# Optimization experiments

Measured on AMD Instinct MI355X. Metric: run time of the kernel, lower is better.

Reference implementation:

```python
import jax, jax.numpy as jnp
import numpy as np

E, K, H, F = 16, 4, 1024, 2048
SL, BS = 2048, 2
ALPHA, LIMIT = 1.702, 7.0
CAPACITY_FACTOR = 1.0


def setup_inputs() -> dict:
    key = jax.random.key(0)
    ks = jax.random.split(key, 7)
    x = jax.random.normal(ks[0], (SL, BS, H), jnp.float32)
    router_weight = jax.random.normal(ks[1], (E, H), jnp.float32) * 0.02
    router_bias = jax.random.normal(ks[2], (E,), jnp.float32) * 0.02
    w1 = jax.random.normal(ks[3], (E, H, 2 * F), jnp.float32) * 0.02
    w2 = jax.random.normal(ks[4], (E, F, H), jnp.float32) * 0.02
    w1_bias = jax.random.normal(ks[5], (E, 2 * F), jnp.float32) * 0.02
    w2_bias = jax.random.normal(ks[6], (E, H), jnp.float32) * 0.02
    return {"x": x, "router_weight": router_weight, "router_bias": router_bias,
            "w1": w1, "w2": w2, "w1_bias": w1_bias, "w2_bias": w2_bias}


def reference(x, router_weight, router_bias, w1, w2, w1_bias, w2_bias):
    sl, bs, h = x.shape
    T = sl * bs                      # total tokens
    N = T * K                        # total routed copies
    C = int(CAPACITY_FACTOR * K * T / E)  # static expert capacity
    xf = x.reshape(T, h)

    # --- route_tokens ---
    logits = xf @ router_weight.T + router_bias            # [T, E]
    expert_weights, expert_indices = jax.lax.top_k(logits, K)  # [T, K]
    expert_weights = jax.nn.softmax(expert_weights, axis=-1)
    router_scores = jnp.zeros_like(logits).at[
        jnp.arange(T)[:, None], expert_indices].set(expert_weights).T  # [E, T]

    # --- indices_and_bins: stable sort by expert + histogram ---
    te = expert_indices.reshape(-1)                        # [N] expert id per copy
    ew = expert_weights.reshape(-1)                        # [N] weight per copy
    order = jnp.argsort(te)                                # stable sort -> permutation
    tokens_per_expert = jnp.zeros((E,), jnp.int32).at[te].add(1)
    starts = jnp.cumsum(tokens_per_expert) - tokens_per_expert  # exclusive cumsum

    # --- binned_gather: [E, C, H], overflow tokens dropped, underfull slots zero ---
    j = jnp.arange(C)
    pos = starts[:, None] + j[None, :]                     # [E, C] position in sorted order
    valid = j[None, :] < tokens_per_expert[:, None]        # [E, C]
    flat_idx = order[jnp.clip(pos, 0, N - 1)]              # [E, C] index into flattened copies
    tok = flat_idx // K                                    # [E, C] source token row
    xb = jnp.where(valid[..., None], xf[tok], 0.0)         # [E, C, H]

    # --- mlp_forward: interleaved GLU ---
    gate_up = jnp.einsum('ech,ehf->ecf', xb, w1) + w1_bias[:, None, :]  # [E, C, 2F]
    gate = jnp.minimum(gate_up[..., ::2], LIMIT)
    up = jnp.clip(gate_up[..., 1::2], -LIMIT, LIMIT)
    glu = gate * jax.nn.sigmoid(gate * ALPHA)
    y = jnp.einsum('ecf,efh->ech', (up + 1.0) * glu, w2) + w2_bias[:, None, :]  # [E, C, H]

    # --- binned_scatter: weighted combine back to token rows ---
    w = jnp.where(valid, ew[flat_idx], 0.0)                # [E, C]
    out = jnp.zeros((T, h), x.dtype).at[tok.reshape(-1)].add(
        (w[..., None] * y).reshape(-1, h))
    return out.reshape(sl, bs, h), expert_weights, router_scores
```

## Files before the change

kernel.cpp:

```cpp
#include <hip/hip_runtime.h>
#include <hip/hip_bf16.h>

#define T_TOK 4096
#define E_EXP 16
#define TOPK 4
#define HDIM 1024
#define FDIM 2048
#define CAP 1024
#define NCOPY (T_TOK*TOPK)

typedef __bf16 bf16x8 __attribute__((ext_vector_type(8)));
typedef __bf16 bf16x4 __attribute__((ext_vector_type(4)));
typedef float  f32x4  __attribute__((ext_vector_type(4)));

__global__ __launch_bounds__(64) void router_kernel(
    const float* __restrict__ x, const float* __restrict__ rw, const float* __restrict__ rb,
    float* __restrict__ ew_out, float* __restrict__ rs_out, int* __restrict__ te_out)
{
    int t = blockIdx.x;
    int lane = threadIdx.x;
    const float* xr = x + (size_t)t * HDIM;
    float xv[16];
#pragma unroll
    for (int i = 0; i < 16; ++i) xv[i] = xr[i * 64 + lane];
    float lg[E_EXP];
#pragma unroll
    for (int e = 0; e < E_EXP; ++e) {
        const float* wrow = rw + (size_t)e * HDIM;
        float s = 0.f;
#pragma unroll
        for (int i = 0; i < 16; ++i) s += xv[i] * wrow[i * 64 + lane];
#pragma unroll
        for (int off = 32; off > 0; off >>= 1) s += __shfl_xor(s, off, 64);
        lg[e] = s + rb[e];
    }
    int mask = 0; float vals[4]; int idxs[4];
#pragma unroll
    for (int k = 0; k < 4; ++k) {
        float m = -3.4e38f; int a = 0;
#pragma unroll
        for (int e = 0; e < E_EXP; ++e) {
            bool take = (((mask >> e) & 1) == 0) && (lg[e] > m);
            m = take ? lg[e] : m;
            a = take ? e : a;
        }
        vals[k] = m; idxs[k] = a; mask |= (1 << a);
    }
    float wk[4]; float ssum = 0.f;
#pragma unroll
    for (int k = 0; k < 4; ++k) { wk[k] = __expf(vals[k] - vals[0]); ssum += wk[k]; }
    float inv = 1.f / ssum;
#pragma unroll
    for (int k = 0; k < 4; ++k) wk[k] *= inv;
    if (lane < 4) {
        float wv = 0.f; int iv = 0;
#pragma unroll
        for (int k = 0; k < 4; ++k) if (lane == k) { wv = wk[k]; iv = idxs[k]; }
        ew_out[t * 4 + lane] = wv;
        te_out[t * 4 + lane] = iv;
    }
    if (lane < E_EXP) {
        float v = 0.f;
#pragma unroll
        for (int k = 0; k < 4; ++k) v = (idxs[k] == lane) ? wk[k] : v;
        rs_out[(size_t)lane * T_TOK + t] = v;
    }
}

__global__ __launch_bounds__(256) void binning_kernel(
    const int* __restrict__ te, const float* __restrict__ ew,
    int* __restrict__ slot_tok, float* __restrict__ slot_w)
{
    __shared__ int cnt[256][17];
    int tid = threadIdx.x;
#pragma unroll
    for (int e = 0; e < E_EXP; ++e) cnt[tid][e] = 0;
    __syncthreads();
    int base = tid * 64;
    for (int i = 0; i < 64; ++i) cnt[tid][te[base + i]]++;
    __syncthreads();
    if (tid < E_EXP) {
        int run = 0;
        for (int t2 = 0; t2 < 256; ++t2) { int v = cnt[t2][tid]; cnt[t2][tid] = run; run += v; }
    }
    __syncthreads();
    for (int s = tid; s < E_EXP * CAP; s += 256) { slot_tok[s] = -1; slot_w[s] = 0.f; }
    __syncthreads();
    for (int i = 0; i < 64; ++i) {
        int idx = base + i;
        int e = te[idx];
        int r = cnt[tid][e]; cnt[tid][e] = r + 1;
        if (r < CAP) { slot_tok[e * CAP + r] = idx >> 2; slot_w[e * CAP + r] = ew[idx]; }
    }
}

__global__ __launch_bounds__(256) void gather_kernel(
    const float* __restrict__ x, const int* __restrict__ slot_tok, __bf16* __restrict__ xg)
{
    int s = blockIdx.x, tid = threadIdx.x;
    int tok = slot_tok[s];
    bf16x4 o;
    if (tok >= 0) {
        float4 v = *(const float4*)(x + (size_t)tok * HDIM + tid * 4);
        o[0] = (__bf16)v.x; o[1] = (__bf16)v.y; o[2] = (__bf16)v.z; o[3] = (__bf16)v.w;
    } else {
        o[0] = (__bf16)0.f; o[1] = (__bf16)0.f; o[2] = (__bf16)0.f; o[3] = (__bf16)0.f;
    }
    *(bf16x4*)(xg + (size_t)s * HDIM + tid * 4) = o;
}

__global__ __launch_bounds__(256) void transpose_cvt_kernel(
    const float* __restrict__ in, __bf16* __restrict__ out, int R, int Cc, int tilesR, int tilesC)
{
    __shared__ __bf16 tile[64][68];
    int bx = blockIdx.x;
    int tpe = tilesR * tilesC;
    int e = bx / tpe; int rem = bx - e * tpe;
    int tr = rem / tilesC; int tc = rem - tr * tilesC;
    const float* ine = in + (size_t)e * R * Cc;
    __bf16* oute = out + (size_t)e * R * Cc;
    int r0 = tr * 64, c0 = tc * 64;
    int tid = threadIdx.x;
    int rr = tid >> 4, c4 = (tid & 15) << 2;
#pragma unroll
    for (int it = 0; it < 4; ++it) {
        int r = rr + it * 16;
        float4 v = *(const float4*)(ine + (size_t)(r0 + r) * Cc + c0 + c4);
        tile[r][c4 + 0] = (__bf16)v.x; tile[r][c4 + 1] = (__bf16)v.y;
        tile[r][c4 + 2] = (__bf16)v.z; tile[r][c4 + 3] = (__bf16)v.w;
    }
    __syncthreads();
#pragma unroll
    for (int it = 0; it < 4; ++it) {
        int c = rr + it * 16;
        bf16x4 o;
        o[0] = tile[c4 + 0][c]; o[1] = tile[c4 + 1][c];
        o[2] = tile[c4 + 2][c]; o[3] = tile[c4 + 3][c];
        *(bf16x4*)(oute + (size_t)(c0 + c) * R + r0 + c4) = o;
    }
}

__global__ __launch_bounds__(256) void zero_kernel(float4* p)
{
    p[(size_t)blockIdx.x * 256 + threadIdx.x] = make_float4(0.f, 0.f, 0.f, 0.f);
}

template <int EPI>
__global__ __launch_bounds__(256) void gemm_kernel(
    const __bf16* __restrict__ A, const __bf16* __restrict__ Bt, const float* __restrict__ bias,
    __bf16* __restrict__ actout, float* __restrict__ out,
    const int* __restrict__ slot_tok, const float* __restrict__ slot_w,
    int Kd, int tilesM, int tilesN, int N)
{
    __shared__ __bf16 at[128 * 32];
    __shared__ __bf16 bts[128 * 32];
    int bx = blockIdx.x;
    int tpe = tilesM * tilesN;
    int e = bx / tpe; int rem = bx - e * tpe;
    int bm = rem / tilesN; int bn = rem - bm * tilesN;
    const __bf16* Ab = A + (size_t)e * 1024 * Kd + (size_t)(bm * 128) * Kd;
    const __bf16* Bb = Bt + (size_t)e * N * Kd + (size_t)(bn * 128) * Kd;
    int tid = threadIdx.x;
    int c0 = tid, c1 = tid + 256;
    int ar0 = c0 >> 2, ak0 = (c0 & 3) << 3;
    int ar1 = c1 >> 2, ak1 = (c1 & 3) << 3;

    uint4 ra0 = *(const uint4*)(Ab + (size_t)ar0 * Kd + ak0);
    uint4 ra1 = *(const uint4*)(Ab + (size_t)ar1 * Kd + ak1);
    uint4 rb0 = *(const uint4*)(Bb + (size_t)ar0 * Kd + ak0);
    uint4 rb1 = *(const uint4*)(Bb + (size_t)ar1 * Kd + ak1);

    f32x4 zero4 = {0.f, 0.f, 0.f, 0.f};
    f32x4 acc[4][4];
#pragma unroll
    for (int mi = 0; mi < 4; ++mi)
#pragma unroll
        for (int ni = 0; ni < 4; ++ni) acc[mi][ni] = zero4;

    int w = tid >> 6, l = tid & 63;
    int q = l >> 4, ln = l & 15;
    int wr = (w >> 1) << 6, wc = (w & 1) << 6;

    for (int k0 = 0; k0 < Kd; k0 += 32) {
        *(uint4*)(at + c0 * 8) = ra0;
        *(uint4*)(at + c1 * 8) = ra1;
        *(uint4*)(bts + c0 * 8) = rb0;
        *(uint4*)(bts + c1 * 8) = rb1;
        int kn = k0 + 32;
        if (kn < Kd) {
            ra0 = *(const uint4*)(Ab + (size_t)ar0 * Kd + kn + ak0);
            ra1 = *(const uint4*)(Ab + (size_t)ar1 * Kd + kn + ak1);
            rb0 = *(const uint4*)(Bb + (size_t)ar0 * Kd + kn + ak0);
            rb1 = *(const uint4*)(Bb + (size_t)ar1 * Kd + kn + ak1);
        }
        __syncthreads();
        bf16x8 af[4], bfr[4];
#pragma unroll
        for (int mi = 0; mi < 4; ++mi)
            af[mi] = *(const bf16x8*)(at + (wr + mi * 16 + ln) * 32 + q * 8);
#pragma unroll
        for (int ni = 0; ni < 4; ++ni)
            bfr[ni] = *(const bf16x8*)(bts + (wc + ni * 16 + ln) * 32 + q * 8);
#pragma unroll
        for (int mi = 0; mi < 4; ++mi)
#pragma unroll
            for (int ni = 0; ni < 4; ++ni)
                acc[mi][ni] = __builtin_amdgcn_mfma_f32_16x16x32_bf16(af[mi], bfr[ni], acc[mi][ni], 0, 0, 0);
        __syncthreads();
    }

    float bv[4];
#pragma unroll
    for (int ni = 0; ni < 4; ++ni) bv[ni] = bias[(size_t)e * N + bn * 128 + wc + ni * 16 + ln];

    if constexpr (EPI == 0) {
        __bf16* act_e = actout + (size_t)e * 1024 * FDIM;
#pragma unroll
        for (int mi = 0; mi < 4; ++mi)
#pragma unroll
            for (int ni = 0; ni < 4; ++ni)
#pragma unroll
                for (int r = 0; r < 4; ++r) {
                    int m = bm * 128 + wr + mi * 16 + q * 4 + r;
                    int n = bn * 128 + wc + ni * 16 + ln;
                    float v = acc[mi][ni][r] + bv[ni];
                    float o = __shfl_xor(v, 1, 64);
                    float gate = (ln & 1) ? o : v;
                    float up   = (ln & 1) ? v : o;
                    gate = fminf(gate, 7.f);
                    up = fminf(fmaxf(up, -7.f), 7.f);
                    float glu = gate / (1.f + __expf(-1.702f * gate));
                    float a = (up + 1.f) * glu;
                    if ((ln & 1) == 0) act_e[(size_t)m * FDIM + (n >> 1)] = (__bf16)a;
                }
    } else {
#pragma unroll
        for (int mi = 0; mi < 4; ++mi)
#pragma unroll
            for (int r = 0; r < 4; ++r) {
                int m = bm * 128 + wr + mi * 16 + q * 4 + r;
                int tok = slot_tok[e * CAP + m];
                float wgt = slot_w[e * CAP + m];
                if (tok >= 0) {
#pragma unroll
                    for (int ni = 0; ni < 4; ++ni) {
                        int n = bn * 128 + wc + ni * 16 + ln;
                        float v = (acc[mi][ni][r] + bv[ni]) * wgt;
                        unsafeAtomicAdd(out + (size_t)tok * HDIM + n, v);
                    }
                }
            }
    }
}

extern "C" void kernel_launch(void* const* d_in, const int* in_sizes, int n_in,
                              void* d_out, int out_size, void* d_ws, size_t ws_size,
                              hipStream_t stream)
{
    const float* x  = (const float*)d_in[0];
    const float* rw = (const float*)d_in[1];
    const float* rb = (const float*)d_in[2];
    const float* w1 = (const float*)d_in[3];
    const float* w2 = (const float*)d_in[4];
    const float* b1 = (const float*)d_in[5];
    const float* b2 = (const float*)d_in[6];
    float* out_main = (float*)d_out;
    float* ew_out = out_main + (size_t)T_TOK * HDIM;
    float* rs_out = ew_out + (size_t)T_TOK * TOPK;

    char* ws = (char*)d_ws;
    size_t off = 0;
    auto alloc = [&](size_t bytes) { void* p = ws + off; off += (bytes + 255) & ~(size_t)255; return p; };
    __bf16* w1t = (__bf16*)alloc((size_t)E_EXP * 2 * FDIM * HDIM * 2);
    __bf16* w2t = (__bf16*)alloc((size_t)E_EXP * HDIM * FDIM * 2);
    __bf16* xg  = (__bf16*)alloc((size_t)E_EXP * CAP * HDIM * 2);
    __bf16* act = (__bf16*)alloc((size_t)E_EXP * CAP * FDIM * 2);
    int*   te       = (int*)alloc((size_t)NCOPY * 4);
    int*   slot_tok = (int*)alloc((size_t)E_EXP * CAP * 4);
    float* slot_w   = (float*)alloc((size_t)E_EXP * CAP * 4);

    zero_kernel<<<(T_TOK * HDIM) / 1024, 256, 0, stream>>>((float4*)out_main);
    router_kernel<<<T_TOK, 64, 0, stream>>>(x, rw, rb, ew_out, rs_out, te);
    binning_kernel<<<1, 256, 0, stream>>>(te, ew_out, slot_tok, slot_w);
    gather_kernel<<<E_EXP * CAP, 256, 0, stream>>>(x, slot_tok, xg);
    transpose_cvt_kernel<<<E_EXP * (HDIM / 64) * (2 * FDIM / 64), 256, 0, stream>>>(
        w1, w1t, HDIM, 2 * FDIM, HDIM / 64, 2 * FDIM / 64);
    transpose_cvt_kernel<<<E_EXP * (FDIM / 64) * (HDIM / 64), 256, 0, stream>>>(
        w2, w2t, FDIM, HDIM, FDIM / 64, HDIM / 64);
    gemm_kernel<0><<<E_EXP * 8 * 32, 256, 0, stream>>>(
        xg, w1t, b1, act, nullptr, nullptr, nullptr, HDIM, 8, 32, 2 * FDIM);
    gemm_kernel<1><<<E_EXP * 8 * 8, 256, 0, stream>>>(
        act, w2t, b2, nullptr, out_main, slot_tok, slot_w, FDIM, 8, 8, HDIM);
}
```

Baseline: 912.1 us.

## Double-buffer GEMM LDS tiles using direct global-to-LDS async loads

Replaces the register-staged global loads followed by LDS stores in the expert GEMM with direct global_load_lds transfers into a double-buffered shared-memory tile. The next K-slice is fetched into the alternate buffer while MFMAs consume the current one, and one barrier per iteration is removed. The intent is to cut VGPR pressure and LDS write instructions and to overlap memory with compute. It doubles LDS use per block. It also relies on the barrier to cover async LDS writes; without an explicit vmcnt wait this may be a correctness risk.

```diff
diff --git a/kernel.cpp b/kernel.cpp
--- a/kernel.cpp
+++ b/kernel.cpp
@@ -12,6 +12,13 @@
 typedef __bf16 bf16x8 __attribute__((ext_vector_type(8)));
 typedef __bf16 bf16x4 __attribute__((ext_vector_type(4)));
 typedef float  f32x4  __attribute__((ext_vector_type(4)));
+
+__device__ __forceinline__ void gload_lds16(const __bf16* g, __bf16* l)
+{
+    __builtin_amdgcn_global_load_lds(
+        (__attribute__((address_space(1))) void*)g,
+        (__attribute__((address_space(3))) void*)l, 16, 0, 0);
+}
 
 __global__ __launch_bounds__(64) void router_kernel(
     const float* __restrict__ x, const float* __restrict__ rw, const float* __restrict__ rb,
@@ -152,8 +159,8 @@
     const int* __restrict__ slot_tok, const float* __restrict__ slot_w,
     int Kd, int tilesM, int tilesN, int N)
 {
-    __shared__ __bf16 at[128 * 32];
-    __shared__ __bf16 bts[128 * 32];
+    __shared__ __bf16 at[2][128 * 32];
+    __shared__ __bf16 bts[2][128 * 32];
     int bx = blockIdx.x;
     int tpe = tilesM * tilesN;
     int e = bx / tpe; int rem = bx - e * tpe;
@@ -161,14 +168,11 @@
     const __bf16* Ab = A + (size_t)e * 1024 * Kd + (size_t)(bm * 128) * Kd;
     const __bf16* Bb = Bt + (size_t)e * N * Kd + (size_t)(bn * 128) * Kd;
     int tid = threadIdx.x;
-    int c0 = tid, c1 = tid + 256;
-    int ar0 = c0 >> 2, ak0 = (c0 & 3) << 3;
-    int ar1 = c1 >> 2, ak1 = (c1 & 3) << 3;
-
-    uint4 ra0 = *(const uint4*)(Ab + (size_t)ar0 * Kd + ak0);
-    uint4 ra1 = *(const uint4*)(Ab + (size_t)ar1 * Kd + ak1);
-    uint4 rb0 = *(const uint4*)(Bb + (size_t)ar0 * Kd + ak0);
-    uint4 rb1 = *(const uint4*)(Bb + (size_t)ar1 * Kd + ak1);
+    int ar0 = tid >> 2, ak0 = (tid & 3) << 3;
+    const __bf16* ga0 = Ab + (size_t)ar0 * Kd + ak0;
+    const __bf16* ga1 = ga0 + (size_t)64 * Kd;
+    const __bf16* gb0 = Bb + (size_t)ar0 * Kd + ak0;
+    const __bf16* gb1 = gb0 + (size_t)64 * Kd;
 
     f32x4 zero4 = {0.f, 0.f, 0.f, 0.f};
     f32x4 acc[4][4];
@@ -181,32 +185,36 @@
     int q = l >> 4, ln = l & 15;
     int wr = (w >> 1) << 6, wc = (w & 1) << 6;
 
-    for (int k0 = 0; k0 < Kd; k0 += 32) {
-        *(uint4*)(at + c0 * 8) = ra0;
-        *(uint4*)(at + c1 * 8) = ra1;
-        *(uint4*)(bts + c0 * 8) = rb0;
-        *(uint4*)(bts + c1 * 8) = rb1;
-        int kn = k0 + 32;
-        if (kn < Kd) {
-            ra0 = *(const uint4*)(Ab + (size_t)ar0 * Kd + kn + ak0);
-            ra1 = *(const uint4*)(Ab + (size_t)ar1 * Kd + kn + ak1);
-            rb0 = *(const uint4*)(Bb + (size_t)ar0 * Kd + kn + ak0);
-            rb1 = *(const uint4*)(Bb + (size_t)ar1 * Kd + kn + ak1);
+    int nk = Kd >> 5;
+    gload_lds16(ga0, &at[0][tid * 8]);
+    gload_lds16(ga1, &at[0][(tid + 256) * 8]);
+    gload_lds16(gb0, &bts[0][tid * 8]);
+    gload_lds16(gb1, &bts[0][(tid + 256) * 8]);
+    __syncthreads();
+
+    int cur = 0;
+    for (int t = 0; t < nk; ++t) {
+        if (t + 1 < nk) {
+            int ko = (t + 1) << 5;
+            gload_lds16(ga0 + ko, &at[cur ^ 1][tid * 8]);
+            gload_lds16(ga1 + ko, &at[cur ^ 1][(tid + 256) * 8]);
+            gload_lds16(gb0 + ko, &bts[cur ^ 1][tid * 8]);
+            gload_lds16(gb1 + ko, &bts[cur ^ 1][(tid + 256) * 8]);
         }
-        __syncthreads();
         bf16x8 af[4], bfr[4];
 #pragma unroll
         for (int mi = 0; mi < 4; ++mi)
-            af[mi] = *(const bf16x8*)(at + (wr + mi * 16 + ln) * 32 + q * 8);
+            af[mi] = *(const bf16x8*)(&at[cur][(wr + mi * 16 + ln) * 32 + q * 8]);
 #pragma unroll
         for (int ni = 0; ni < 4; ++ni)
-            bfr[ni] = *(const bf16x8*)(bts + (wc + ni * 16 + ln) * 32 + q * 8);
+            bfr[ni] = *(const bf16x8*)(&bts[cur][(wc + ni * 16 + ln) * 32 + q * 8]);
 #pragma unroll
         for (int mi = 0; mi < 4; ++mi)
 #pragma unroll
             for (int ni = 0; ni < 4; ++ni)
                 acc[mi][ni] = __builtin_amdgcn_mfma_f32_16x16x32_bf16(af[mi], bfr[ni], acc[mi][ni], 0, 0, 0);
         __syncthreads();
+        cur ^= 1;
     }
 
     float bv[4];
```

New measurement: 952.9 us. 1.04x slower.

## Replace atomic scatter-add with dense expert output buffer and gather-combine kernel

Applied to the files above, without the earlier changes.

The second GEMM now writes unweighted expert outputs densely into a scratch buffer that reuses the w1 transposed workspace. A new combine kernel then gathers each token's four copies via a per-copy slot map and applies the routing weights. This removes the zero-fill kernel and the fp32 atomic adds to the output, at the cost of an extra 64MB write and read round trip through the scratch buffer and one more launch.

```diff
diff --git a/kernel.cpp b/kernel.cpp
--- a/kernel.cpp
+++ b/kernel.cpp
@@ -68,8 +68,8 @@
 }
 
 __global__ __launch_bounds__(256) void binning_kernel(
-    const int* __restrict__ te, const float* __restrict__ ew,
-    int* __restrict__ slot_tok, float* __restrict__ slot_w)
+    const int* __restrict__ te,
+    int* __restrict__ slot_tok, int* __restrict__ copy_slot)
 {
     __shared__ int cnt[256][17];
     int tid = threadIdx.x;
@@ -84,13 +84,14 @@
         for (int t2 = 0; t2 < 256; ++t2) { int v = cnt[t2][tid]; cnt[t2][tid] = run; run += v; }
     }
     __syncthreads();
-    for (int s = tid; s < E_EXP * CAP; s += 256) { slot_tok[s] = -1; slot_w[s] = 0.f; }
+    for (int s = tid; s < E_EXP * CAP; s += 256) slot_tok[s] = -1;
     __syncthreads();
     for (int i = 0; i < 64; ++i) {
         int idx = base + i;
         int e = te[idx];
         int r = cnt[tid][e]; cnt[tid][e] = r + 1;
-        if (r < CAP) { slot_tok[e * CAP + r] = idx >> 2; slot_w[e * CAP + r] = ew[idx]; }
+        if (r < CAP) { slot_tok[e * CAP + r] = idx >> 2; copy_slot[idx] = e * CAP + r; }
+        else copy_slot[idx] = -1;
     }
 }
 
@@ -140,16 +141,29 @@
     }
 }
 
-__global__ __launch_bounds__(256) void zero_kernel(float4* p)
-{
-    p[(size_t)blockIdx.x * 256 + threadIdx.x] = make_float4(0.f, 0.f, 0.f, 0.f);
+__global__ __launch_bounds__(256) void combine_kernel(
+    const float* __restrict__ ybuf, const float* __restrict__ ew,
+    const int* __restrict__ copy_slot, float* __restrict__ out)
+{
+    int t = blockIdx.x, tid = threadIdx.x;
+    float4 acc = make_float4(0.f, 0.f, 0.f, 0.f);
+#pragma unroll
+    for (int k = 0; k < 4; ++k) {
+        int s = copy_slot[t * 4 + k];
+        float wk = ew[t * 4 + k];
+        if (s >= 0) {
+            float4 v = *(const float4*)(ybuf + (size_t)s * HDIM + tid * 4);
+            acc.x += wk * v.x; acc.y += wk * v.y;
+            acc.z += wk * v.z; acc.w += wk * v.w;
+        }
+    }
+    *(float4*)(out + (size_t)t * HDIM + tid * 4) = acc;
 }
 
 template <int EPI>
 __global__ __launch_bounds__(256) void gemm_kernel(
     const __bf16* __restrict__ A, const __bf16* __restrict__ Bt, const float* __restrict__ bias,
     __bf16* __restrict__ actout, float* __restrict__ out,
-    const int* __restrict__ slot_tok, const float* __restrict__ slot_w,
     int Kd, int tilesM, int tilesN, int N)
 {
     __shared__ __bf16 at[128 * 32];
@@ -234,20 +248,16 @@
                     if ((ln & 1) == 0) act_e[(size_t)m * FDIM + (n >> 1)] = (__bf16)a;
                 }
     } else {
+        float* ye = out + (size_t)e * CAP * N;
 #pragma unroll
         for (int mi = 0; mi < 4; ++mi)
 #pragma unroll
             for (int r = 0; r < 4; ++r) {
                 int m = bm * 128 + wr + mi * 16 + q * 4 + r;
-                int tok = slot_tok[e * CAP + m];
-                float wgt = slot_w[e * CAP + m];
-                if (tok >= 0) {
-#pragma unroll
-                    for (int ni = 0; ni < 4; ++ni) {
-                        int n = bn * 128 + wc + ni * 16 + ln;
-                        float v = (acc[mi][ni][r] + bv[ni]) * wgt;
-                        unsafeAtomicAdd(out + (size_t)tok * HDIM + n, v);
-                    }
+#pragma unroll
+                for (int ni = 0; ni < 4; ++ni) {
+                    int n = bn * 128 + wc + ni * 16 + ln;
+                    ye[(size_t)m * N + n] = acc[mi][ni][r] + bv[ni];
                 }
             }
     }
@@ -277,18 +287,19 @@
     __bf16* act = (__bf16*)alloc((size_t)E_EXP * CAP * FDIM * 2);
     int*   te       = (int*)alloc((size_t)NCOPY * 4);
     int*   slot_tok = (int*)alloc((size_t)E_EXP * CAP * 4);
-    float* slot_w   = (float*)alloc((size_t)E_EXP * CAP * 4);
-
-    zero_kernel<<<(T_TOK * HDIM) / 1024, 256, 0, stream>>>((float4*)out_main);
+    int*   copy_slot= (int*)alloc((size_t)NCOPY * 4);
+    float* ybuf = (float*)w1t;
+
     router_kernel<<<T_TOK, 64, 0, stream>>>(x, rw, rb, ew_out, rs_out, te);
-    binning_kernel<<<1, 256, 0, stream>>>(te, ew_out, slot_tok, slot_w);
+    binning_kernel<<<1, 256, 0, stream>>>(te, slot_tok, copy_slot);
     gather_kernel<<<E_EXP * CAP, 256, 0, stream>>>(x, slot_tok, xg);
     transpose_cvt_kernel<<<E_EXP * (HDIM / 64) * (2 * FDIM / 64), 256, 0, stream>>>(
         w1, w1t, HDIM, 2 * FDIM, HDIM / 64, 2 * FDIM / 64);
     transpose_cvt_kernel<<<E_EXP * (FDIM / 64) * (HDIM / 64), 256, 0, stream>>>(
         w2, w2t, FDIM, HDIM, FDIM / 64, HDIM / 64);
     gemm_kernel<0><<<E_EXP * 8 * 32, 256, 0, stream>>>(
-        xg, w1t, b1, act, nullptr, nullptr, nullptr, HDIM, 8, 32, 2 * FDIM);
+        xg, w1t, b1, act, nullptr, HDIM, 8, 32, 2 * FDIM);
     gemm_kernel<1><<<E_EXP * 8 * 8, 256, 0, stream>>>(
-        act, w2t, b2, nullptr, out_main, slot_tok, slot_w, FDIM, 8, 8, HDIM);
-}
+        act, w2t, b2, nullptr, ybuf, FDIM, 8, 8, HDIM);
+    combine_kernel<<<T_TOK, 256, 0, stream>>>(ybuf, ew_out, copy_slot, out_main);
+}
```

Measured after the change: 874.6 us. 4.1% less time.
